# Kernel tuning notes

Measured on AMD Instinct MI355X. Metric: run time of the kernel, lower is better.

Reference implementation:

```python
import jax, jax.numpy as jnp
import numpy as np

IDIM1, IDIM2, HDIM = 512, 512, 256
EPS = 1e-5

def _layernorm(x, g, b):
    mu = jnp.mean(x, axis=-1, keepdims=True)
    var = jnp.var(x, axis=-1, keepdims=True)
    return (x - mu) * jax.lax.rsqrt(var + EPS) * g + b

def setup_inputs() -> dict:
    key = jax.random.key(0)
    ks = jax.random.split(key, 8)
    B, N, T = 16, 32, 256
    s1 = 1.0 / np.sqrt(IDIM1)
    s2 = 1.0 / np.sqrt(IDIM2)
    s3 = 1.0 / np.sqrt(HDIM)
    return {
        "x1": jax.random.normal(ks[0], (B, N, IDIM1), jnp.float32),
        "x2": jax.random.normal(ks[1], (B, T, IDIM2), jnp.float32),
        "W1": jax.random.uniform(ks[2], (IDIM1, HDIM), jnp.float32, -s1, s1),
        "b1": jax.random.uniform(ks[3], (HDIM,), jnp.float32, -s1, s1),
        "W2": jax.random.uniform(ks[4], (IDIM2, HDIM), jnp.float32, -s2, s2),
        "b2": jax.random.uniform(ks[5], (HDIM,), jnp.float32, -s2, s2),
        "W3": jax.random.uniform(ks[6], (HDIM, HDIM), jnp.float32, -s3, s3),
        "b3": jax.random.uniform(ks[7], (HDIM,), jnp.float32, -s3, s3),
        "g_norm": jnp.ones((HDIM,), jnp.float32),
        "be_norm": jnp.zeros((HDIM,), jnp.float32),
        "g_norm1": jnp.ones((HDIM,), jnp.float32),
        "be_norm1": jnp.zeros((HDIM,), jnp.float32),
    }

def reference(x1, x2, W1, b1, W2, b2, W3, b3, g_norm, be_norm, g_norm1, be_norm1):
    h1 = jax.nn.relu(x1 @ W1 + b1)          # [B,N,H]
    h2 = jax.nn.relu(x2 @ W2 + b2)          # [B,T,H]
    x = h1[:, :, None, :] * h2[:, None, :, :]  # [B,N,T,H] broadcast Hadamard
    x = _layernorm(x, g_norm, be_norm)
    x = x @ W3 + b3
    return jax.nn.relu(_layernorm(x, g_norm1, be_norm1))
```

## Files before the change

kernel.cpp:

```cpp
#include <hip/hip_runtime.h>
#include <hip/hip_bf16.h>
#include <stdint.h>

#define BB 16
#define NN 32
#define TT 256
#define HH 256
#define DD 512
#define EPSF 1e-5f

#define TROWS 32
#define ROWB  512

typedef __attribute__((ext_vector_type(8))) short short8;
typedef __attribute__((ext_vector_type(4))) float floatx4;

__device__ __forceinline__ unsigned short f2bf(float f) {
    union { float f; unsigned u; } v; v.f = f;
    unsigned u = v.u;
    unsigned r = u + 0x7FFFu + ((u >> 16) & 1u);
    return (unsigned short)(r >> 16);
}
__device__ __forceinline__ float bf2f(unsigned short h) {
    union { unsigned u; float f; } v; v.u = ((unsigned)h) << 16;
    return v.f;
}

__device__ __forceinline__ void split2(float f0, float f1, unsigned& hp, unsigned& lp) {
    union { float f; unsigned u; } a0, a1, r0, r1;
    a0.f = f0; a1.f = f1;
    const unsigned h0 = a0.u & 0xFFFF0000u;
    const unsigned h1 = a1.u & 0xFFFF0000u;
    union { unsigned u; float f; } b0, b1;
    b0.u = h0; b1.u = h1;
    r0.f = f0 - b0.f;
    r1.f = f1 - b1.f;
    hp = (a0.u >> 16) | h1;
    lp = (r0.u >> 16) | (r1.u & 0xFFFF0000u);
}

__global__ __launch_bounds__(256) void prep_kernel(
    const float* __restrict__ x1, const float* __restrict__ x2,
    const float* __restrict__ W1, const float* __restrict__ b1,
    const float* __restrict__ W2, const float* __restrict__ b2,
    const float* __restrict__ W3,
    float* __restrict__ h1, float* __restrict__ h2,
    unsigned short* __restrict__ W3p_hi, unsigned short* __restrict__ W3p_lo)
{
    const int blk = blockIdx.x;
    const int tid = threadIdx.x;

    if (blk >= 1152) {
        const int p  = (blk - 1152) * 256 + tid;
        const int o0 = p * 16;
        unsigned short thi[16], tlo[16];
#pragma unroll
        for (int e = 0; e < 16; ++e) {
            const int o    = o0 + e;
            const int j    = o & 7;
            const int lane = (o >> 3) & 63;
            const int kk   = (o >> 9) & 7;
            const int ct   = o >> 12;
            const int krow = kk * 32 + (lane >> 4) * 8 + j;
            const int col  = ct * 16 + (lane & 15);
            const float w  = W3[krow * HH + col];
            const unsigned short hi = f2bf(w);
            thi[e] = hi;
            tlo[e] = f2bf(w - bf2f(hi));
        }
        unsigned wh[8], wl[8];
#pragma unroll
        for (int e = 0; e < 8; ++e) {
            wh[e] = (unsigned)thi[2 * e] | ((unsigned)thi[2 * e + 1] << 16);
            wl[e] = (unsigned)tlo[2 * e] | ((unsigned)tlo[2 * e + 1] << 16);
        }
        uint4* dh = reinterpret_cast<uint4*>(W3p_hi + o0);
        dh[0] = make_uint4(wh[0], wh[1], wh[2], wh[3]);
        dh[1] = make_uint4(wh[4], wh[5], wh[6], wh[7]);
        uint4* dl = reinterpret_cast<uint4*>(W3p_lo + o0);
        dl[0] = make_uint4(wl[0], wl[1], wl[2], wl[3]);
        dl[1] = make_uint4(wl[4], wl[5], wl[6], wl[7]);
        return;
    }

    __shared__ float xs[8][DD];

    const int rowgrp  = blk >> 1;
    const int colbase = (blk & 1) * 128;

    const float* x; const float* W; const float* bias; float* h; int row0;
    if (rowgrp < 64) { x = x1; W = W1; bias = b1; h = h1; row0 = rowgrp * 8; }
    else             { x = x2; W = W2; bias = b2; h = h2; row0 = (rowgrp - 64) * 8; }

    {
        const float4* xg = reinterpret_cast<const float4*>(x + (size_t)row0 * DD);
        float4* xl = reinterpret_cast<float4*>(&xs[0][0]);
#pragma unroll
        for (int i = 0; i < 4; ++i) xl[tid + 256 * i] = xg[tid + 256 * i];
    }
    __syncthreads();

    const int jj  = tid & 127;
    const int rh  = tid >> 7;
    const int col = colbase + jj;

    float acc[4] = {0.0f, 0.0f, 0.0f, 0.0f};
    const float* Wp = W + col;

    for (int k = 0; k < DD; k += 8) {
        float w[8];
#pragma unroll
        for (int q = 0; q < 8; ++q) w[q] = Wp[(size_t)(k + q) * HH];
#pragma unroll
        for (int r = 0; r < 4; ++r) {
            const float4 xa = *reinterpret_cast<const float4*>(&xs[rh * 4 + r][k]);
            const float4 xb = *reinterpret_cast<const float4*>(&xs[rh * 4 + r][k + 4]);
            float s = acc[r];
            s = fmaf(xa.x, w[0], s); s = fmaf(xa.y, w[1], s);
            s = fmaf(xa.z, w[2], s); s = fmaf(xa.w, w[3], s);
            s = fmaf(xb.x, w[4], s); s = fmaf(xb.y, w[5], s);
            s = fmaf(xb.z, w[6], s); s = fmaf(xb.w, w[7], s);
            acc[r] = s;
        }
    }

    const float bb = bias[col];
#pragma unroll
    for (int r = 0; r < 4; ++r) {
        const float v = acc[r] + bb;
        h[(size_t)(row0 + rh * 4 + r) * HH + col] = v > 0.0f ? v : 0.0f;
    }
}

__global__ __launch_bounds__(256, 5) void fused_mfma_kernel(
    const float* __restrict__ h1, const float* __restrict__ h2,
    const unsigned short* __restrict__ W3p_hi,
    const unsigned short* __restrict__ W3p_lo,
    const float* __restrict__ b3,
    const float* __restrict__ g0, const float* __restrict__ be0,
    const float* __restrict__ g1, const float* __restrict__ be1,
    float* __restrict__ out)
{
    __shared__ __align__(16) unsigned short Ah_s[TROWS * 256];
    __shared__ __align__(16) unsigned short Al_s[TROWS * 256];

    const int tid  = threadIdx.x;
    const int wave = tid >> 6;
    const int lane = tid & 63;
    const int blk  = blockIdx.x;
    const int tile = blk & 7;
    const int n    = (blk >> 3) & 31;
    const int b    = blk >> 8;

    {
        const float* h1row = h1 + ((size_t)b * NN + n) * HH;
        const float4 h1v  = *reinterpret_cast<const float4*>(h1row + 4 * lane);
        const float4 g0v  = *reinterpret_cast<const float4*>(g0  + 4 * lane);
        const float4 be0v = *reinterpret_cast<const float4*>(be0 + 4 * lane);
        const float* h2b  = h2 + ((size_t)b * TT + tile * TROWS) * HH;

#pragma unroll
        for (int half = 0; half < 2; ++half) {
            float4 v[4]; float s[4], q[4];
#pragma unroll
            for (int i = 0; i < 4; ++i) {
                const int r = wave * 8 + half * 4 + i;
                v[i] = *reinterpret_cast<const float4*>(h2b + (size_t)r * HH + 4 * lane);
                v[i].x *= h1v.x; v[i].y *= h1v.y; v[i].z *= h1v.z; v[i].w *= h1v.w;
                s[i] = v[i].x + v[i].y + v[i].z + v[i].w;
                q[i] = v[i].x * v[i].x + v[i].y * v[i].y
                     + v[i].z * v[i].z + v[i].w * v[i].w;
            }
#pragma unroll
            for (int off = 32; off >= 1; off >>= 1) {
#pragma unroll
                for (int i = 0; i < 4; ++i) {
                    s[i] += __shfl_xor(s[i], off, 64);
                    q[i] += __shfl_xor(q[i], off, 64);
                }
            }
#pragma unroll
            for (int i = 0; i < 4; ++i) {
                const int r = wave * 8 + half * 4 + i;
                const float mu  = s[i] * (1.0f / HH);
                const float var = q[i] * (1.0f / HH) - mu * mu;
                const float rs  = rsqrtf(var + EPSF);
                float af0 = (v[i].x - mu) * rs * g0v.x + be0v.x;
                float af1 = (v[i].y - mu) * rs * g0v.y + be0v.y;
                float af2 = (v[i].z - mu) * rs * g0v.z + be0v.z;
                float af3 = (v[i].w - mu) * rs * g0v.w + be0v.w;
                unsigned hp0, lp0, hp1, lp1;
                split2(af0, af1, hp0, lp0);
                split2(af2, af3, hp1, lp1);
                const int byteoff = (lane * 8) ^ ((r & 7) << 4);
                *reinterpret_cast<uint2*>(
                    reinterpret_cast<char*>(Ah_s) + r * ROWB + byteoff)
                    = make_uint2(hp0, hp1);
                *reinterpret_cast<uint2*>(
                    reinterpret_cast<char*>(Al_s) + r * ROWB + byteoff)
                    = make_uint2(lp0, lp1);
            }
        }
    }
    __syncthreads();

    const int m  = lane & 15;
    const int qd = lane >> 4;

    floatx4 acc[2][4];
#pragma unroll
    for (int ct = 0; ct < 4; ++ct) {
        const float bv = b3[wave * 64 + ct * 16 + m];
#pragma unroll
        for (int rt = 0; rt < 2; ++rt) {
            acc[rt][ct][0] = bv; acc[rt][ct][1] = bv;
            acc[rt][ct][2] = bv; acc[rt][ct][3] = bv;
        }
    }

    const char* AhB = reinterpret_cast<const char*>(Ah_s);
    const char* AlB = reinterpret_cast<const char*>(Al_s);

#pragma unroll 2
    for (int kk = 0; kk < 8; ++kk) {
        short8 bh[4], bl[4];
#pragma unroll
        for (int ct = 0; ct < 4; ++ct) {
            const size_t off = ((size_t)((wave * 4 + ct) * 8 + kk) * 64 + lane) * 8;
            bh[ct] = *reinterpret_cast<const short8*>(W3p_hi + off);
            bl[ct] = *reinterpret_cast<const short8*>(W3p_lo + off);
        }
        const int swzoff = (kk * 64 + qd * 16) ^ ((m & 7) << 4);
#pragma unroll
        for (int rt = 0; rt < 2; ++rt) {
            const int rowbyte = (rt * 16 + m) * ROWB;
            const short8 ah = *reinterpret_cast<const short8*>(AhB + rowbyte + swzoff);
            const short8 al = *reinterpret_cast<const short8*>(AlB + rowbyte + swzoff);
#pragma unroll
            for (int ct = 0; ct < 4; ++ct) {
                floatx4 c = acc[rt][ct];
                c = __builtin_amdgcn_mfma_f32_16x16x32_bf16(ah, bh[ct], c, 0, 0, 0);
                c = __builtin_amdgcn_mfma_f32_16x16x32_bf16(al, bh[ct], c, 0, 0, 0);
                c = __builtin_amdgcn_mfma_f32_16x16x32_bf16(ah, bl[ct], c, 0, 0, 0);
                acc[rt][ct] = c;
            }
        }
    }

    float ssum[8], qsum[8];
    {
#pragma unroll
        for (int rt = 0; rt < 2; ++rt)
#pragma unroll
            for (int reg = 0; reg < 4; ++reg) {
                float s = 0.0f, q = 0.0f;
#pragma unroll
                for (int ct = 0; ct < 4; ++ct) {
                    const float y = acc[rt][ct][reg];
                    s += y; q = fmaf(y, y, q);
                }
                ssum[rt * 4 + reg] = s; qsum[rt * 4 + reg] = q;
            }
#pragma unroll
        for (int off = 1; off < 16; off <<= 1) {
#pragma unroll
            for (int e = 0; e < 8; ++e) {
                ssum[e] += __shfl_xor(ssum[e], off, 64);
                qsum[e] += __shfl_xor(qsum[e], off, 64);
            }
        }
    }

    __syncthreads();
    float2* Spart = reinterpret_cast<float2*>(Ah_s);
    float2* LNP   = reinterpret_cast<float2*>(Al_s);

    if (m == 0) {
#pragma unroll
        for (int rt = 0; rt < 2; ++rt)
#pragma unroll
            for (int reg = 0; reg < 4; ++reg) {
                const int row = rt * 16 + qd * 4 + reg;
                Spart[row * 4 + wave] = make_float2(ssum[rt * 4 + reg], qsum[rt * 4 + reg]);
            }
    }
    __syncthreads();

    if (tid < TROWS) {
        float s = 0.0f, q = 0.0f;
#pragma unroll
        for (int w = 0; w < 4; ++w) {
            const float2 p = Spart[tid * 4 + w];
            s += p.x; q += p.y;
        }
        const float mu  = s * (1.0f / HH);
        const float var = q * (1.0f / HH) - mu * mu;
        LNP[tid] = make_float2(mu, rsqrtf(var + EPSF));
    }
    __syncthreads();

    {
        const int colb = wave * 64;
        float g1c[4], be1c[4];
#pragma unroll
        for (int ct = 0; ct < 4; ++ct) {
            g1c[ct]  = g1[colb + ct * 16 + m];
            be1c[ct] = be1[colb + ct * 16 + m];
        }
        float* outb = out + (((size_t)b * NN + n) * TT + tile * TROWS) * HH;

#pragma unroll
        for (int rt = 0; rt < 2; ++rt)
#pragma unroll
            for (int reg = 0; reg < 4; ++reg) {
                const int row = rt * 16 + qd * 4 + reg;
                const float2 p = LNP[row];
#pragma unroll
                for (int ct = 0; ct < 4; ++ct) {
                    const float y = acc[rt][ct][reg];
                    const float o = fmaxf((y - p.x) * p.y * g1c[ct] + be1c[ct], 0.0f);
                    outb[(size_t)row * HH + colb + ct * 16 + m] = o;
                }
            }
    }
}

extern "C" void kernel_launch(void* const* d_in, const int* in_sizes, int n_in,
                              void* d_out, int out_size, void* d_ws, size_t ws_size,
                              hipStream_t stream) {
    const float* x1  = (const float*)d_in[0];
    const float* x2  = (const float*)d_in[1];
    const float* W1  = (const float*)d_in[2];
    const float* b1  = (const float*)d_in[3];
    const float* W2  = (const float*)d_in[4];
    const float* b2  = (const float*)d_in[5];
    const float* W3  = (const float*)d_in[6];
    const float* b3  = (const float*)d_in[7];
    const float* g0  = (const float*)d_in[8];
    const float* be0 = (const float*)d_in[9];
    const float* g1  = (const float*)d_in[10];
    const float* be1 = (const float*)d_in[11];
    float* out = (float*)d_out;

    float* h1 = (float*)d_ws;
    float* h2 = h1 + (size_t)BB * NN * HH;
    unsigned short* W3p_hi = (unsigned short*)(h2 + (size_t)BB * TT * HH);
    unsigned short* W3p_lo = W3p_hi + (size_t)HH * HH;

    hipLaunchKernelGGL(prep_kernel, dim3(1168), dim3(256), 0, stream,
                       x1, x2, W1, b1, W2, b2, W3, h1, h2, W3p_hi, W3p_lo);

    hipLaunchKernelGGL(fused_mfma_kernel, dim3(4096), dim3(256), 0, stream,
                       h1, h2, W3p_hi, W3p_lo, b3, g0, be0, g1, be1, out);
}
```

Before: 262.3 us.

## Double the row tile per block and prefetch W3 fragments one k-step ahead

Each block now processes 64 rows of T instead of 32, so every W3 fragment loaded from global memory feeds twice as many MFMAs and the grid halves to 2048 blocks. The W3 loop is fully unrolled and double-buffered, loading the next k-step's fragments while the current one computes. The launch-bounds occupancy hint is removed. In exchange the accumulator and register footprint doubles and shared memory doubles to 64KB, which lowers occupancy, and the grid may no longer fill the GPU as evenly.

```diff
diff --git a/kernel.cpp b/kernel.cpp
--- a/kernel.cpp
+++ b/kernel.cpp
@@ -9,7 +9,7 @@
 #define DD 512
 #define EPSF 1e-5f
 
-#define TROWS 32
+#define TROWS 64
 #define ROWB  512
 
 typedef __attribute__((ext_vector_type(8))) short short8;
@@ -132,7 +132,7 @@
     }
 }
 
-__global__ __launch_bounds__(256, 5) void fused_mfma_kernel(
+__global__ __launch_bounds__(256) void fused_mfma_kernel(
     const float* __restrict__ h1, const float* __restrict__ h2,
     const unsigned short* __restrict__ W3p_hi,
     const unsigned short* __restrict__ W3p_lo,
@@ -148,9 +148,9 @@
     const int wave = tid >> 6;
     const int lane = tid & 63;
     const int blk  = blockIdx.x;
-    const int tile = blk & 7;
-    const int n    = (blk >> 3) & 31;
-    const int b    = blk >> 8;
+    const int tile = blk & 3;
+    const int n    = (blk >> 2) & 31;
+    const int b    = blk >> 7;
 
     {
         const float* h1row = h1 + ((size_t)b * NN + n) * HH;
@@ -160,11 +160,11 @@
         const float* h2b  = h2 + ((size_t)b * TT + tile * TROWS) * HH;
 
 #pragma unroll
-        for (int half = 0; half < 2; ++half) {
+        for (int batch = 0; batch < 4; ++batch) {
             float4 v[4]; float s[4], q[4];
 #pragma unroll
             for (int i = 0; i < 4; ++i) {
-                const int r = wave * 8 + half * 4 + i;
+                const int r = wave * 16 + batch * 4 + i;
                 v[i] = *reinterpret_cast<const float4*>(h2b + (size_t)r * HH + 4 * lane);
                 v[i].x *= h1v.x; v[i].y *= h1v.y; v[i].z *= h1v.z; v[i].w *= h1v.w;
                 s[i] = v[i].x + v[i].y + v[i].z + v[i].w;
@@ -181,7 +181,7 @@
             }
 #pragma unroll
             for (int i = 0; i < 4; ++i) {
-                const int r = wave * 8 + half * 4 + i;
+                const int r = wave * 16 + batch * 4 + i;
                 const float mu  = s[i] * (1.0f / HH);
                 const float var = q[i] * (1.0f / HH) - mu * mu;
                 const float rs  = rsqrtf(var + EPSF);
@@ -207,12 +207,12 @@
     const int m  = lane & 15;
     const int qd = lane >> 4;
 
-    floatx4 acc[2][4];
+    floatx4 acc[4][4];
 #pragma unroll
     for (int ct = 0; ct < 4; ++ct) {
         const float bv = b3[wave * 64 + ct * 16 + m];
 #pragma unroll
-        for (int rt = 0; rt < 2; ++rt) {
+        for (int rt = 0; rt < 4; ++rt) {
             acc[rt][ct][0] = bv; acc[rt][ct][1] = bv;
             acc[rt][ct][2] = bv; acc[rt][ct][3] = bv;
         }
@@ -221,36 +221,47 @@
     const char* AhB = reinterpret_cast<const char*>(Ah_s);
     const char* AlB = reinterpret_cast<const char*>(Al_s);
 
-#pragma unroll 2
+    short8 bhA[4], blA[4], bhB[4], blB[4];
+#pragma unroll
+    for (int ct = 0; ct < 4; ++ct) {
+        const size_t off = ((size_t)((wave * 4 + ct) * 8 + 0) * 64 + lane) * 8;
+        bhA[ct] = *reinterpret_cast<const short8*>(W3p_hi + off);
+        blA[ct] = *reinterpret_cast<const short8*>(W3p_lo + off);
+    }
+
+#pragma unroll
     for (int kk = 0; kk < 8; ++kk) {
-        short8 bh[4], bl[4];
-#pragma unroll
-        for (int ct = 0; ct < 4; ++ct) {
-            const size_t off = ((size_t)((wave * 4 + ct) * 8 + kk) * 64 + lane) * 8;
-            bh[ct] = *reinterpret_cast<const short8*>(W3p_hi + off);
-            bl[ct] = *reinterpret_cast<const short8*>(W3p_lo + off);
+        if (kk < 7) {
+#pragma unroll
+            for (int ct = 0; ct < 4; ++ct) {
+                const size_t off = ((size_t)((wave * 4 + ct) * 8 + kk + 1) * 64 + lane) * 8;
+                bhB[ct] = *reinterpret_cast<const short8*>(W3p_hi + off);
+                blB[ct] = *reinterpret_cast<const short8*>(W3p_lo + off);
+            }
         }
         const int swzoff = (kk * 64 + qd * 16) ^ ((m & 7) << 4);
 #pragma unroll
-        for (int rt = 0; rt < 2; ++rt) {
+        for (int rt = 0; rt < 4; ++rt) {
             const int rowbyte = (rt * 16 + m) * ROWB;
             const short8 ah = *reinterpret_cast<const short8*>(AhB + rowbyte + swzoff);
             const short8 al = *reinterpret_cast<const short8*>(AlB + rowbyte + swzoff);
 #pragma unroll
             for (int ct = 0; ct < 4; ++ct) {
                 floatx4 c = acc[rt][ct];
-                c = __builtin_amdgcn_mfma_f32_16x16x32_bf16(ah, bh[ct], c, 0, 0, 0);
-                c = __builtin_amdgcn_mfma_f32_16x16x32_bf16(al, bh[ct], c, 0, 0, 0);
-                c = __builtin_amdgcn_mfma_f32_16x16x32_bf16(ah, bl[ct], c, 0, 0, 0);
+                c = __builtin_amdgcn_mfma_f32_16x16x32_bf16(ah, bhA[ct], c, 0, 0, 0);
+                c = __builtin_amdgcn_mfma_f32_16x16x32_bf16(al, bhA[ct], c, 0, 0, 0);
+                c = __builtin_amdgcn_mfma_f32_16x16x32_bf16(ah, blA[ct], c, 0, 0, 0);
                 acc[rt][ct] = c;
             }
         }
-    }
-
-    float ssum[8], qsum[8];
+#pragma unroll
+        for (int ct = 0; ct < 4; ++ct) { bhA[ct] = bhB[ct]; blA[ct] = blB[ct]; }
+    }
+
+    float ssum[16], qsum[16];
     {
 #pragma unroll
-        for (int rt = 0; rt < 2; ++rt)
+        for (int rt = 0; rt < 4; ++rt)
 #pragma unroll
             for (int reg = 0; reg < 4; ++reg) {
                 float s = 0.0f, q = 0.0f;
@@ -264,7 +275,7 @@
 #pragma unroll
         for (int off = 1; off < 16; off <<= 1) {
 #pragma unroll
-            for (int e = 0; e < 8; ++e) {
+            for (int e = 0; e < 16; ++e) {
                 ssum[e] += __shfl_xor(ssum[e], off, 64);
                 qsum[e] += __shfl_xor(qsum[e], off, 64);
             }
@@ -277,7 +288,7 @@
 
     if (m == 0) {
 #pragma unroll
-        for (int rt = 0; rt < 2; ++rt)
+        for (int rt = 0; rt < 4; ++rt)
 #pragma unroll
             for (int reg = 0; reg < 4; ++reg) {
                 const int row = rt * 16 + qd * 4 + reg;
@@ -310,7 +321,7 @@
         float* outb = out + (((size_t)b * NN + n) * TT + tile * TROWS) * HH;
 
 #pragma unroll
-        for (int rt = 0; rt < 2; ++rt)
+        for (int rt = 0; rt < 4; ++rt)
 #pragma unroll
             for (int reg = 0; reg < 4; ++reg) {
                 const int row = rt * 16 + qd * 4 + reg;
@@ -350,6 +361,6 @@
     hipLaunchKernelGGL(prep_kernel, dim3(1168), dim3(256), 0, stream,
                        x1, x2, W1, b1, W2, b2, W3, h1, h2, W3p_hi, W3p_lo);
 
-    hipLaunchKernelGGL(fused_mfma_kernel, dim3(4096), dim3(256), 0, stream,
+    hipLaunchKernelGGL(fused_mfma_kernel, dim3(2048), dim3(256), 0, stream,
                        h1, h2, W3p_hi, W3p_lo, b3, g0, be0, g1, be1, out);
 }
```

After: 304.6 us. +16.1%, slower.
